# Optimization experiments

Measured on AMD Instinct MI355X. Metric: run time of the kernel, lower is better.

Reference implementation:

```python
import jax, jax.numpy as jnp
import numpy as np

N_NODES = 163840
N_EDGES = 2621440
F_IN = 64
F_HID = 64
SUBG = 20  # size_subgraph_samples
NEG_SLOPE = 0.2


def gat_conv(x, src, dst, W, a_src, a_dst, b):
    """PyG GATConv, heads=1, concat. src/dst already include self-loops."""
    n = x.shape[0]
    h = x @ W                               # [N, H]
    al_s = h @ a_src                        # [N]
    al_d = h @ a_dst                        # [N]
    e = jax.nn.leaky_relu(al_s[src] + al_d[dst], NEG_SLOPE)  # [E]
    # softmax over incoming edges of each dst node
    m = jax.ops.segment_max(e, dst, num_segments=n)
    ex = jnp.exp(e - m[dst])
    denom = jax.ops.segment_sum(ex, dst, num_segments=n)
    alpha = ex / (denom[dst] + 1e-16)
    msg = h[src] * alpha[:, None]           # [E, H]
    out = jax.ops.segment_sum(msg, dst, num_segments=n)
    return out + b


def setup_inputs() -> dict:
    key = jax.random.key(0)
    ks = jax.random.split(key, 12)
    s = 0.05
    return {
        "x": jax.random.normal(ks[0], (N_NODES, F_IN), jnp.float32),
        "edge_index": jax.random.randint(ks[1], (2, N_EDGES), 0, N_NODES, jnp.int64 if jax.config.jax_enable_x64 else jnp.int32),
        "W1": jax.random.normal(ks[2], (F_IN, F_HID), jnp.float32) * s,
        "a_src1": jax.random.normal(ks[3], (F_HID,), jnp.float32) * s,
        "a_dst1": jax.random.normal(ks[4], (F_HID,), jnp.float32) * s,
        "b1": jnp.zeros((F_HID,), jnp.float32),
        "W2": jax.random.normal(ks[5], (F_HID, F_HID), jnp.float32) * s,
        "a_src2": jax.random.normal(ks[6], (F_HID,), jnp.float32) * s,
        "a_dst2": jax.random.normal(ks[7], (F_HID,), jnp.float32) * s,
        "b2": jnp.zeros((F_HID,), jnp.float32),
        "W_out": jax.random.normal(ks[8], (F_HID * SUBG, 1), jnp.float32) * s,
        "b_out": jnp.zeros((1,), jnp.float32),
    }


def reference(x, edge_index, W1, a_src1, a_dst1, b1, W2, a_src2, a_dst2, b2, W_out, b_out):
    n = x.shape[0]
    loop = jnp.arange(n, dtype=edge_index.dtype)
    src = jnp.concatenate([edge_index[0], loop])  # add_self_loops=True
    dst = jnp.concatenate([edge_index[1], loop])
    h = gat_conv(x, src, dst, W1, a_src1, a_dst1, b1)
    h = jax.nn.relu(h)  # dropout is identity in eval mode
    h = gat_conv(h, src, dst, W2, a_src2, a_dst2, b2)
    h = jax.nn.relu(h)
    h = h.reshape(n // SUBG, F_HID * SUBG)
    return h @ W_out + b_out
```

## Files before the change

kernel.cpp:

```cpp
#include <hip/hip_runtime.h>
#include <math.h>

#define F 64
#define NPB 160
#define STAGE_CAP 6304

typedef __attribute__((ext_vector_type(8))) short bf16x8;
typedef __attribute__((ext_vector_type(4))) float f32x4;

__device__ inline unsigned short f2bf(float f) {
  unsigned int u = __float_as_uint(f);
  u += 0x7fffu + ((u >> 16) & 1u);
  return (unsigned short)(u >> 16);
}


__global__ __launch_bounds__(256) void k_bin_count(const int* __restrict__ edst, int* __restrict__ cntT,
                                                   int e, int ch, int nblk, int nb,
                                                   const float* __restrict__ W1, const float* __restrict__ W2,
                                                   uint4* __restrict__ wf) {
  __shared__ int h[1024];
  int k = blockIdx.x, tid = threadIdx.x;
  if (k == nblk) {
    for (int i = tid; i < 1024; i += 256) {
      int layer = i >> 9, rem = i & 511;
      int cb = rem >> 6, lane = rem & 63;
      int c = cb >> 1, kk = cb & 1;
      int l15 = lane & 15, quad = lane >> 4;
      const float* W = layer ? W2 : W1;
      unsigned short p[8];
      #pragma unroll
      for (int j = 0; j < 8; j++) {
        int kd = kk * 32 + quad * 8 + j;
        p[j] = f2bf(W[kd * F + c * 16 + l15]);
      }
      wf[i] = *(const uint4*)p;
    }
    return;
  }
  for (int i = tid; i < nb; i += 256) h[i] = 0;
  __syncthreads();
  int beg = k * ch, end = min(e, beg + ch);
  for (int i = beg + tid; i < end; i += 256) atomicAdd(&h[edst[i] / NPB], 1);
  __syncthreads();
  for (int b = tid; b < nb; b += 256) cntT[b * nblk + k] = h[b];
}

__global__ __launch_bounds__(256) void k_scan1(const int* __restrict__ counts, int* __restrict__ offs,
                                               int* __restrict__ bsums, int n) {
  int tid = threadIdx.x, lane = tid & 63, wv = tid >> 6;
  int i = blockIdx.x * 256 + tid;
  int v = (i < n) ? counts[i] : 0;
  int x = v;
  #pragma unroll
  for (int o = 1; o <= 32; o <<= 1) { int y = __shfl_up(x, o); if (lane >= o) x += y; }
  __shared__ int wsum[4];
  if (lane == 63) wsum[wv] = x;
  __syncthreads();
  int add = 0;
  for (int w = 0; w < wv; w++) add += wsum[w];
  int incl = x + add;
  if (i < n) offs[i] = incl - v;
  if (tid == 255) bsums[blockIdx.x] = incl;
}

__global__ __launch_bounds__(256) void k_scan2(int* __restrict__ bs, int nb,
                                               float* __restrict__ out, const float* __restrict__ bo, int ng) {
  __shared__ int wsum[4];
  __shared__ int carry_sh;
  int tid = threadIdx.x, lane = tid & 63, wv = tid >> 6;
  float b0 = bo[0];
  for (int i = tid; i < ng; i += 256) out[i] = b0;
  if (tid == 0) carry_sh = 0;
  __syncthreads();
  for (int base = 0; base < nb; base += 256) {
    int i = base + tid;
    int v = (i < nb) ? bs[i] : 0;
    int x = v;
    #pragma unroll
    for (int o = 1; o <= 32; o <<= 1) { int y = __shfl_up(x, o); if (lane >= o) x += y; }
    if (lane == 63) wsum[wv] = x;
    __syncthreads();
    int add = 0;
    for (int w = 0; w < wv; w++) add += wsum[w];
    int incl = x + add;
    int carry = carry_sh;
    if (i < nb) bs[i] = incl - v + carry;
    __syncthreads();
    if (tid == 255) carry_sh = carry + incl;
    __syncthreads();
  }
}

__global__ __launch_bounds__(256) void k_bin_scatter(const int* __restrict__ esrc, const int* __restrict__ edst,
                                                     const int* __restrict__ posT, const int* __restrict__ bsums,
                                                     unsigned int* __restrict__ binned,
                                                     int e, int ch, int nblk, int nb) {
  __shared__ int cur[1024];
  int k = blockIdx.x, tid = threadIdx.x;
  for (int b = tid; b < nb; b += 256) {
    int idx = b * nblk + k;
    cur[b] = posT[idx] + bsums[idx >> 8];
  }
  __syncthreads();
  int beg = k * ch, end = min(e, beg + ch);
  for (int i = beg + tid; i < end; i += 256) {
    int d = edst[i];
    int b = d / NPB;
    unsigned int ld = (unsigned int)(d - b * NPB);
    int p = atomicAdd(&cur[b], 1);
    binned[p] = (unsigned int)esrc[i] | (ld << 24);
  }
}

__global__ __launch_bounds__(256) void k_bucket_csr(const unsigned int* __restrict__ binned,
                                                    const int* __restrict__ posT, const int* __restrict__ bsums,
                                                    int* __restrict__ ssrc, int* __restrict__ offs,
                                                    int n, int nblk, int nb, int e) {
  __shared__ int ncnt[NPB];
  __shared__ int noff[NPB];
  __shared__ int cur[NPB];
  __shared__ int sc[256];
  __shared__ int stage[STAGE_CAP];
  int b = blockIdx.x, tid = threadIdx.x;
  int node0 = b * NPB;
  int nn = min(NPB, n - node0);
  int i0 = b * nblk;
  int ebeg = posT[i0] + bsums[i0 >> 8];
  int eend;
  if (b == nb - 1) eend = e;
  else { int i1 = (b + 1) * nblk; eend = posT[i1] + bsums[i1 >> 8]; }
  int ecnt = eend - ebeg;
  for (int i = tid; i < NPB; i += 256) ncnt[i] = 0;
  __syncthreads();
  for (int i = tid; i < ecnt; i += 256) { unsigned int v = binned[ebeg + i]; atomicAdd(&ncnt[v >> 24], 1); }
  __syncthreads();
  int x = (tid < nn) ? ncnt[tid] + 1 : 0;
  sc[tid] = x;
  __syncthreads();
  #pragma unroll
  for (int o = 1; o < 256; o <<= 1) {
    int y = (tid >= o) ? sc[tid - o] : 0;
    __syncthreads();
    sc[tid] += y;
    __syncthreads();
  }
  if (tid < nn) noff[tid] = sc[tid] - x;
  __syncthreads();
  int tot = ecnt + nn;
  int outbase = ebeg + node0;
  bool staged = (tot <= STAGE_CAP);
  if (tid < nn) {
    cur[tid] = noff[tid] + 1;
    offs[node0 + tid] = outbase + noff[tid];
    if (staged) stage[noff[tid]] = node0 + tid;
    else        ssrc[outbase + noff[tid]] = node0 + tid;
  }
  __syncthreads();
  if (staged) {
    for (int i = tid; i < ecnt; i += 256) {
      unsigned int v = binned[ebeg + i];
      int p = atomicAdd(&cur[v >> 24], 1);
      stage[p] = (int)(v & 0xFFFFFFu);
    }
    __syncthreads();
    for (int i = tid; i < tot; i += 256) ssrc[outbase + i] = stage[i];
  } else {
    for (int i = tid; i < ecnt; i += 256) {
      unsigned int v = binned[ebeg + i];
      int p = atomicAdd(&cur[v >> 24], 1);
      ssrc[outbase + p] = (int)(v & 0xFFFFFFu);
    }
  }
  if (b == 0 && tid == 0) offs[n] = e + n;
}

template<bool IN_BF16>
__global__ __launch_bounds__(256) void k_gemm(const void* __restrict__ in, const uint4* __restrict__ wf,
                                              const float* __restrict__ avs, const float* __restrict__ avd,
                                              unsigned short* __restrict__ hgb, float* __restrict__ als,
                                              float* __restrict__ ald, int n) {
  int tid = threadIdx.x, lane = tid & 63, wv = tid >> 6;
  int l15 = lane & 15, quad = lane >> 4;
  bf16x8 bfr[4][2];
  #pragma unroll
  for (int cb = 0; cb < 8; cb++) {
    uint4 u = wf[cb * 64 + lane];
    bfr[cb >> 1][cb & 1] = *(const bf16x8*)&u;
  }
  float as_l[4], ad_l[4];
  #pragma unroll
  for (int c = 0; c < 4; c++) { as_l[c] = avs[c * 16 + l15]; ad_l[c] = avd[c * 16 + l15]; }

  int nchunks = n >> 6;
  for (int chunk = blockIdx.x; chunk < nchunks; chunk += gridDim.x) {
    int r0 = (chunk << 6) + (wv << 4);
    bf16x8 a0, a1;
    if constexpr (IN_BF16) {
      const uint4* row4 = (const uint4*)((const unsigned short*)in + (size_t)(r0 + l15) * F);
      uint4 u0 = row4[quad];
      uint4 u1 = row4[quad + 4];
      a0 = *(const bf16x8*)&u0;
      a1 = *(const bf16x8*)&u1;
    } else {
      const float4* xr = (const float4*)((const float*)in + (size_t)(r0 + l15) * F + quad * 8);
      float4 xa = xr[0], xb = xr[1];
      float4 xc = xr[8], xd = xr[9];
      a0[0] = (short)f2bf(xa.x); a0[1] = (short)f2bf(xa.y); a0[2] = (short)f2bf(xa.z); a0[3] = (short)f2bf(xa.w);
      a0[4] = (short)f2bf(xb.x); a0[5] = (short)f2bf(xb.y); a0[6] = (short)f2bf(xb.z); a0[7] = (short)f2bf(xb.w);
      a1[0] = (short)f2bf(xc.x); a1[1] = (short)f2bf(xc.y); a1[2] = (short)f2bf(xc.z); a1[3] = (short)f2bf(xc.w);
      a1[4] = (short)f2bf(xd.x); a1[5] = (short)f2bf(xd.y); a1[6] = (short)f2bf(xd.z); a1[7] = (short)f2bf(xd.w);
    }
    f32x4 cfr[4];
    #pragma unroll
    for (int c = 0; c < 4; c++) {
      cfr[c] = (f32x4){0.f, 0.f, 0.f, 0.f};
      cfr[c] = __builtin_amdgcn_mfma_f32_16x16x32_bf16(a0, bfr[c][0], cfr[c], 0, 0, 0);
      cfr[c] = __builtin_amdgcn_mfma_f32_16x16x32_bf16(a1, bfr[c][1], cfr[c], 0, 0, 0);
    }
    #pragma unroll
    for (int i = 0; i < 4; i++) {
      int row = r0 + quad * 4 + i;
      #pragma unroll
      for (int c = 0; c < 4; c++) hgb[(size_t)row * F + c * 16 + l15] = f2bf(cfr[c][i]);
      float ps = cfr[0][i] * as_l[0] + cfr[1][i] * as_l[1] + cfr[2][i] * as_l[2] + cfr[3][i] * as_l[3];
      float pd = cfr[0][i] * ad_l[0] + cfr[1][i] * ad_l[1] + cfr[2][i] * ad_l[2] + cfr[3][i] * ad_l[3];
      #pragma unroll
      for (int o = 1; o <= 8; o <<= 1) { ps += __shfl_xor(ps, o); pd += __shfl_xor(pd, o); }
      if (l15 == 0) { als[row] = ps; ald[row] = pd; }
    }
  }
}

template<int MODE>
__global__ __launch_bounds__(256) void k_spmm(const int* __restrict__ offs, const int* __restrict__ ssrc,
                                              const unsigned short* __restrict__ hgb,
                                              const float* __restrict__ als, const float* __restrict__ ald,
                                              const float* __restrict__ bias, const float* __restrict__ Wout,
                                              void* __restrict__ outp, int n) {
  int tid = threadIdx.x, lane = tid & 63, wv = tid >> 6;
  int g8 = lane >> 3, l8 = lane & 7;
  const uint4* hg4 = (const uint4*)hgb;
  float4 bl0 = ((const float4*)bias)[l8 * 2];
  float4 bl1 = ((const float4*)bias)[l8 * 2 + 1];

  int node = (blockIdx.x * 4 + wv) * 8 + g8;
  int cnode = min(node, n - 1);
  bool nodeok = node < n;
  int beg = offs[cnode];
  int deg = nodeok ? (offs[cnode + 1] - beg) : 0;
  int degc = max(deg - 1, 0);
  float aldv = ald[cnode];

  int dm = deg;
  #pragma unroll
  for (int o = 8; o <= 32; o <<= 1) dm = max(dm, __shfl_xor(dm, o));

  float s = 0.f;
  float acc[8];
  #pragma unroll
  for (int k = 0; k < 8; k++) acc[k] = 0.f;

  #pragma unroll 2
  for (int j = 0; j < dm; j++) {
    int jj = min(j, degc);
    int src = ssrc[beg + jj];
    float t = als[src] + aldv;
    t = fmaxf(t, 0.2f * t);
    float ex = (j < deg) ? __expf(t) : 0.f;
    s += ex;
    uint4 u = hg4[(size_t)src * 8 + l8];
    acc[0] = fmaf(ex, __uint_as_float(u.x << 16), acc[0]);
    acc[1] = fmaf(ex, __uint_as_float(u.x & 0xffff0000u), acc[1]);
    acc[2] = fmaf(ex, __uint_as_float(u.y << 16), acc[2]);
    acc[3] = fmaf(ex, __uint_as_float(u.y & 0xffff0000u), acc[3]);
    acc[4] = fmaf(ex, __uint_as_float(u.z << 16), acc[4]);
    acc[5] = fmaf(ex, __uint_as_float(u.z & 0xffff0000u), acc[5]);
    acc[6] = fmaf(ex, __uint_as_float(u.w << 16), acc[6]);
    acc[7] = fmaf(ex, __uint_as_float(u.w & 0xffff0000u), acc[7]);
  }

  if (!nodeok) return;
  float iv = 1.f / (s + 1e-16f);
  float r[8];
  r[0] = fmaxf(fmaf(acc[0], iv, bl0.x), 0.f);
  r[1] = fmaxf(fmaf(acc[1], iv, bl0.y), 0.f);
  r[2] = fmaxf(fmaf(acc[2], iv, bl0.z), 0.f);
  r[3] = fmaxf(fmaf(acc[3], iv, bl0.w), 0.f);
  r[4] = fmaxf(fmaf(acc[4], iv, bl1.x), 0.f);
  r[5] = fmaxf(fmaf(acc[5], iv, bl1.y), 0.f);
  r[6] = fmaxf(fmaf(acc[6], iv, bl1.z), 0.f);
  r[7] = fmaxf(fmaf(acc[7], iv, bl1.w), 0.f);
  if constexpr (MODE == 0) {
    unsigned short p[8];
    #pragma unroll
    for (int k = 0; k < 8; k++) p[k] = f2bf(r[k]);
    ((uint4*)outp)[(size_t)node * 8 + l8] = *(const uint4*)p;
  } else {
    int grp = node / 20, slot = node - grp * 20;
    const float* wr = Wout + slot * F + l8 * 8;
    float dot = 0.f;
    #pragma unroll
    for (int k = 0; k < 8; k++) dot = fmaf(r[k], wr[k], dot);
    #pragma unroll
    for (int o = 1; o <= 4; o <<= 1) dot += __shfl_xor(dot, o);
    if (l8 == 0) atomicAdd((float*)outp + grp, dot);
  }
}

extern "C" void kernel_launch(void* const* d_in, const int* in_sizes, int n_in,
                              void* d_out, int out_size, void* d_ws, size_t ws_size,
                              hipStream_t stream) {
  const float* x   = (const float*)d_in[0];
  const int*   ei  = (const int*)d_in[1];
  const float* W1  = (const float*)d_in[2];
  const float* as1 = (const float*)d_in[3];
  const float* ad1 = (const float*)d_in[4];
  const float* b1  = (const float*)d_in[5];
  const float* W2  = (const float*)d_in[6];
  const float* as2 = (const float*)d_in[7];
  const float* ad2 = (const float*)d_in[8];
  const float* b2  = (const float*)d_in[9];
  const float* Wo  = (const float*)d_in[10];
  const float* bo  = (const float*)d_in[11];
  float* out = (float*)d_out;

  const int N = in_sizes[0] / F;
  const int E = in_sizes[1] / 2;
  const int* esrc = ei;
  const int* edst = ei + E;

  size_t off = 0;
  auto alloc = [&](size_t bytes) -> void* {
    void* p = (char*)d_ws + off;
    off += (bytes + 255) & ~(size_t)255;
    return p;
  };
  float* A    = (float*)alloc((size_t)N * F * 4);
  unsigned short* hgb = (unsigned short*)alloc((size_t)N * F * 2);
  float* als  = (float*)alloc((size_t)N * 4);
  float* ald  = (float*)alloc((size_t)N * 4);
  int* offs   = (int*)alloc((size_t)(N + 1) * 4);
  int* bsums  = (int*)alloc(8192);
  int* ssrc   = (int*)alloc((size_t)(E + N) * 4);
  uint4* wf   = (uint4*)alloc(16384);
  (void)ws_size; (void)n_in; (void)out_size;

  const int NBLK = 256;
  const int NB = (N + NPB - 1) / NPB;
  const int CH = (E + NBLK - 1) / NBLK;
  const int FLAT = NB * NBLK;

  int* cntT = (int*)A;
  int* posT = (int*)((char*)A + ((size_t)FLAT * 4 + 1024));
  unsigned int* binned = (unsigned int*)hgb;

  int gF = (FLAT + 255) / 256;
  int NG = N / 20;

  k_bin_count<<<NBLK + 1, 256, 0, stream>>>(edst, cntT, E, CH, NBLK, NB, W1, W2, wf);
  k_scan1<<<gF, 256, 0, stream>>>(cntT, posT, bsums, FLAT);
  k_scan2<<<1, 256, 0, stream>>>(bsums, gF, out, bo, NG);
  k_bin_scatter<<<NBLK, 256, 0, stream>>>(esrc, edst, posT, bsums, binned, E, CH, NBLK, NB);
  k_bucket_csr<<<NB, 256, 0, stream>>>(binned, posT, bsums, ssrc, offs, N, NBLK, NB, E);

  int gSp = (N + 31) / 32;
  k_gemm<false><<<2560, 256, 0, stream>>>(x, wf, as1, ad1, hgb, als, ald, N);
  k_spmm<0><<<gSp, 256, 0, stream>>>(offs, ssrc, hgb, als, ald, b1, nullptr, A, N);
  k_gemm<true><<<2560, 256, 0, stream>>>(A, wf + 512, as2, ad2, hgb, als, ald, N);
  k_spmm<1><<<gSp, 256, 0, stream>>>(offs, ssrc, hgb, als, ald, b2, Wo, out, N);
}
```

Measured before the change: 319.6 us.

## Fuse layer-1 GEMM into bin scatter and aggregate output atomics in shared memory

The layer-1 feature GEMM now runs in the same launch as the edge bin-scatter: the first blocks scatter edges and the extra blocks compute the GEMM. The binned edge buffer moves out of hgb into a separate region of A so the two can run side by side. The final SpMM sums the Wout dot products per subgraph group in shared memory before issuing a few global atomics, instead of one global atomic per node. The GEMM grids are also resized to one block per 64-row chunk. This removes a kernel launch and most global atomics, at the cost of extra block syncs and a dependence on the new buffer layout fitting inside A.

```diff
diff --git a/kernel.cpp b/kernel.cpp
--- a/kernel.cpp
+++ b/kernel.cpp
@@ -92,25 +92,97 @@
   }
 }
 
-__global__ __launch_bounds__(256) void k_bin_scatter(const int* __restrict__ esrc, const int* __restrict__ edst,
-                                                     const int* __restrict__ posT, const int* __restrict__ bsums,
-                                                     unsigned int* __restrict__ binned,
-                                                     int e, int ch, int nblk, int nb) {
-  __shared__ int cur[1024];
+template<bool IN_BF16>
+__device__ __forceinline__ void gemm_body(const void* __restrict__ in, const uint4* __restrict__ wf,
+                                          const float* __restrict__ avs, const float* __restrict__ avd,
+                                          unsigned short* __restrict__ hgb, float* __restrict__ als,
+                                          float* __restrict__ ald, int n, int bid, int nbl) {
+  int tid = threadIdx.x, lane = tid & 63, wv = tid >> 6;
+  int l15 = lane & 15, quad = lane >> 4;
+  bf16x8 bfr[4][2];
+  #pragma unroll
+  for (int cb = 0; cb < 8; cb++) {
+    uint4 u = wf[cb * 64 + lane];
+    bfr[cb >> 1][cb & 1] = *(const bf16x8*)&u;
+  }
+  float as_l[4], ad_l[4];
+  #pragma unroll
+  for (int c = 0; c < 4; c++) { as_l[c] = avs[c * 16 + l15]; ad_l[c] = avd[c * 16 + l15]; }
+
+  int nchunks = n >> 6;
+  for (int chunk = bid; chunk < nchunks; chunk += nbl) {
+    int r0 = (chunk << 6) + (wv << 4);
+    bf16x8 a0, a1;
+    if constexpr (IN_BF16) {
+      const uint4* row4 = (const uint4*)((const unsigned short*)in + (size_t)(r0 + l15) * F);
+      uint4 u0 = row4[quad];
+      uint4 u1 = row4[quad + 4];
+      a0 = *(const bf16x8*)&u0;
+      a1 = *(const bf16x8*)&u1;
+    } else {
+      const float4* xr = (const float4*)((const float*)in + (size_t)(r0 + l15) * F + quad * 8);
+      float4 xa = xr[0], xb = xr[1];
+      float4 xc = xr[8], xd = xr[9];
+      a0[0] = (short)f2bf(xa.x); a0[1] = (short)f2bf(xa.y); a0[2] = (short)f2bf(xa.z); a0[3] = (short)f2bf(xa.w);
+      a0[4] = (short)f2bf(xb.x); a0[5] = (short)f2bf(xb.y); a0[6] = (short)f2bf(xb.z); a0[7] = (short)f2bf(xb.w);
+      a1[0] = (short)f2bf(xc.x); a1[1] = (short)f2bf(xc.y); a1[2] = (short)f2bf(xc.z); a1[3] = (short)f2bf(xc.w);
+      a1[4] = (short)f2bf(xd.x); a1[5] = (short)f2bf(xd.y); a1[6] = (short)f2bf(xd.z); a1[7] = (short)f2bf(xd.w);
+    }
+    f32x4 cfr[4];
+    #pragma unroll
+    for (int c = 0; c < 4; c++) {
+      cfr[c] = (f32x4){0.f, 0.f, 0.f, 0.f};
+      cfr[c] = __builtin_amdgcn_mfma_f32_16x16x32_bf16(a0, bfr[c][0], cfr[c], 0, 0, 0);
+      cfr[c] = __builtin_amdgcn_mfma_f32_16x16x32_bf16(a1, bfr[c][1], cfr[c], 0, 0, 0);
+    }
+    #pragma unroll
+    for (int i = 0; i < 4; i++) {
+      int row = r0 + quad * 4 + i;
+      #pragma unroll
+      for (int c = 0; c < 4; c++) hgb[(size_t)row * F + c * 16 + l15] = f2bf(cfr[c][i]);
+      float ps = cfr[0][i] * as_l[0] + cfr[1][i] * as_l[1] + cfr[2][i] * as_l[2] + cfr[3][i] * as_l[3];
+      float pd = cfr[0][i] * ad_l[0] + cfr[1][i] * ad_l[1] + cfr[2][i] * ad_l[2] + cfr[3][i] * ad_l[3];
+      #pragma unroll
+      for (int o = 1; o <= 8; o <<= 1) { ps += __shfl_xor(ps, o); pd += __shfl_xor(pd, o); }
+      if (l15 == 0) { als[row] = ps; ald[row] = pd; }
+    }
+  }
+}
+
+__global__ __launch_bounds__(256) void k_scatter_gemm1(const int* __restrict__ esrc, const int* __restrict__ edst,
+                                                       const int* __restrict__ posT, const int* __restrict__ bsums,
+                                                       unsigned int* __restrict__ binned,
+                                                       int e, int ch, int nblk, int nb,
+                                                       const float* __restrict__ x, const uint4* __restrict__ wf,
+                                                       const float* __restrict__ avs, const float* __restrict__ avd,
+                                                       unsigned short* __restrict__ hgb, float* __restrict__ als,
+                                                       float* __restrict__ ald, int n) {
   int k = blockIdx.x, tid = threadIdx.x;
-  for (int b = tid; b < nb; b += 256) {
-    int idx = b * nblk + k;
-    cur[b] = posT[idx] + bsums[idx >> 8];
-  }
-  __syncthreads();
-  int beg = k * ch, end = min(e, beg + ch);
-  for (int i = beg + tid; i < end; i += 256) {
-    int d = edst[i];
-    int b = d / NPB;
-    unsigned int ld = (unsigned int)(d - b * NPB);
-    int p = atomicAdd(&cur[b], 1);
-    binned[p] = (unsigned int)esrc[i] | (ld << 24);
-  }
+  if (k < nblk) {
+    __shared__ int cur[1024];
+    for (int b = tid; b < nb; b += 256) {
+      int idx = b * nblk + k;
+      cur[b] = posT[idx] + bsums[idx >> 8];
+    }
+    __syncthreads();
+    int beg = k * ch, end = min(e, beg + ch);
+    for (int i = beg + tid; i < end; i += 256) {
+      int d = edst[i];
+      int b = d / NPB;
+      unsigned int ld = (unsigned int)(d - b * NPB);
+      int p = atomicAdd(&cur[b], 1);
+      binned[p] = (unsigned int)esrc[i] | (ld << 24);
+    }
+    return;
+  }
+  gemm_body<false>(x, wf, avs, avd, hgb, als, ald, n, k - nblk, (int)gridDim.x - nblk);
+}
+
+__global__ __launch_bounds__(256) void k_gemm2(const unsigned short* __restrict__ in, const uint4* __restrict__ wf,
+                                               const float* __restrict__ avs, const float* __restrict__ avd,
+                                               unsigned short* __restrict__ hgb, float* __restrict__ als,
+                                               float* __restrict__ ald, int n) {
+  gemm_body<true>(in, wf, avs, avd, hgb, als, ald, n, blockIdx.x, gridDim.x);
 }
 
 __global__ __launch_bounds__(256) void k_bucket_csr(const unsigned int* __restrict__ binned,
@@ -175,63 +247,6 @@
   if (b == 0 && tid == 0) offs[n] = e + n;
 }
 
-template<bool IN_BF16>
-__global__ __launch_bounds__(256) void k_gemm(const void* __restrict__ in, const uint4* __restrict__ wf,
-                                              const float* __restrict__ avs, const float* __restrict__ avd,
-                                              unsigned short* __restrict__ hgb, float* __restrict__ als,
-                                              float* __restrict__ ald, int n) {
-  int tid = threadIdx.x, lane = tid & 63, wv = tid >> 6;
-  int l15 = lane & 15, quad = lane >> 4;
-  bf16x8 bfr[4][2];
-  #pragma unroll
-  for (int cb = 0; cb < 8; cb++) {
-    uint4 u = wf[cb * 64 + lane];
-    bfr[cb >> 1][cb & 1] = *(const bf16x8*)&u;
-  }
-  float as_l[4], ad_l[4];
-  #pragma unroll
-  for (int c = 0; c < 4; c++) { as_l[c] = avs[c * 16 + l15]; ad_l[c] = avd[c * 16 + l15]; }
-
-  int nchunks = n >> 6;
-  for (int chunk = blockIdx.x; chunk < nchunks; chunk += gridDim.x) {
-    int r0 = (chunk << 6) + (wv << 4);
-    bf16x8 a0, a1;
-    if constexpr (IN_BF16) {
-      const uint4* row4 = (const uint4*)((const unsigned short*)in + (size_t)(r0 + l15) * F);
-      uint4 u0 = row4[quad];
-      uint4 u1 = row4[quad + 4];
-      a0 = *(const bf16x8*)&u0;
-      a1 = *(const bf16x8*)&u1;
-    } else {
-      const float4* xr = (const float4*)((const float*)in + (size_t)(r0 + l15) * F + quad * 8);
-      float4 xa = xr[0], xb = xr[1];
-      float4 xc = xr[8], xd = xr[9];
-      a0[0] = (short)f2bf(xa.x); a0[1] = (short)f2bf(xa.y); a0[2] = (short)f2bf(xa.z); a0[3] = (short)f2bf(xa.w);
-      a0[4] = (short)f2bf(xb.x); a0[5] = (short)f2bf(xb.y); a0[6] = (short)f2bf(xb.z); a0[7] = (short)f2bf(xb.w);
-      a1[0] = (short)f2bf(xc.x); a1[1] = (short)f2bf(xc.y); a1[2] = (short)f2bf(xc.z); a1[3] = (short)f2bf(xc.w);
-      a1[4] = (short)f2bf(xd.x); a1[5] = (short)f2bf(xd.y); a1[6] = (short)f2bf(xd.z); a1[7] = (short)f2bf(xd.w);
-    }
-    f32x4 cfr[4];
-    #pragma unroll
-    for (int c = 0; c < 4; c++) {
-      cfr[c] = (f32x4){0.f, 0.f, 0.f, 0.f};
-      cfr[c] = __builtin_amdgcn_mfma_f32_16x16x32_bf16(a0, bfr[c][0], cfr[c], 0, 0, 0);
-      cfr[c] = __builtin_amdgcn_mfma_f32_16x16x32_bf16(a1, bfr[c][1], cfr[c], 0, 0, 0);
-    }
-    #pragma unroll
-    for (int i = 0; i < 4; i++) {
-      int row = r0 + quad * 4 + i;
-      #pragma unroll
-      for (int c = 0; c < 4; c++) hgb[(size_t)row * F + c * 16 + l15] = f2bf(cfr[c][i]);
-      float ps = cfr[0][i] * as_l[0] + cfr[1][i] * as_l[1] + cfr[2][i] * as_l[2] + cfr[3][i] * as_l[3];
-      float pd = cfr[0][i] * ad_l[0] + cfr[1][i] * ad_l[1] + cfr[2][i] * ad_l[2] + cfr[3][i] * ad_l[3];
-      #pragma unroll
-      for (int o = 1; o <= 8; o <<= 1) { ps += __shfl_xor(ps, o); pd += __shfl_xor(pd, o); }
-      if (l15 == 0) { als[row] = ps; ald[row] = pd; }
-    }
-  }
-}
-
 template<int MODE>
 __global__ __launch_bounds__(256) void k_spmm(const int* __restrict__ offs, const int* __restrict__ ssrc,
                                               const unsigned short* __restrict__ hgb,
@@ -243,6 +258,9 @@
   const uint4* hg4 = (const uint4*)hgb;
   float4 bl0 = ((const float4*)bias)[l8 * 2];
   float4 bl1 = ((const float4*)bias)[l8 * 2 + 1];
+
+  __shared__ float gsl[3];
+  if (MODE == 1 && tid < 3) gsl[tid] = 0.f;
 
   int node = (blockIdx.x * 4 + wv) * 8 + g8;
   int cnode = min(node, n - 1);
@@ -280,7 +298,6 @@
     acc[7] = fmaf(ex, __uint_as_float(u.w & 0xffff0000u), acc[7]);
   }
 
-  if (!nodeok) return;
   float iv = 1.f / (s + 1e-16f);
   float r[8];
   r[0] = fmaxf(fmaf(acc[0], iv, bl0.x), 0.f);
@@ -291,20 +308,30 @@
   r[5] = fmaxf(fmaf(acc[5], iv, bl1.y), 0.f);
   r[6] = fmaxf(fmaf(acc[6], iv, bl1.z), 0.f);
   r[7] = fmaxf(fmaf(acc[7], iv, bl1.w), 0.f);
+
   if constexpr (MODE == 0) {
+    if (!nodeok) return;
     unsigned short p[8];
     #pragma unroll
     for (int k = 0; k < 8; k++) p[k] = f2bf(r[k]);
     ((uint4*)outp)[(size_t)node * 8 + l8] = *(const uint4*)p;
   } else {
-    int grp = node / 20, slot = node - grp * 20;
+    int node0 = blockIdx.x * 32;
+    int grp0 = node0 / 20;
+    int grp = cnode / 20, slot = cnode - grp * 20;
     const float* wr = Wout + slot * F + l8 * 8;
     float dot = 0.f;
     #pragma unroll
     for (int k = 0; k < 8; k++) dot = fmaf(r[k], wr[k], dot);
     #pragma unroll
     for (int o = 1; o <= 4; o <<= 1) dot += __shfl_xor(dot, o);
-    if (l8 == 0) atomicAdd((float*)outp + grp, dot);
+    __syncthreads();
+    if (nodeok && l8 == 0) atomicAdd(&gsl[grp - grp0], dot);
+    __syncthreads();
+    if (tid < 3) {
+      float v = gsl[tid];
+      if (v != 0.f) atomicAdd((float*)outp + grp0 + tid, v);
+    }
   }
 }
 
@@ -353,7 +380,7 @@
 
   int* cntT = (int*)A;
   int* posT = (int*)((char*)A + ((size_t)FLAT * 4 + 1024));
-  unsigned int* binned = (unsigned int*)hgb;
+  unsigned int* binned = (unsigned int*)((char*)A + (size_t)8 * 1024 * 1024);
 
   int gF = (FLAT + 255) / 256;
   int NG = N / 20;
@@ -361,12 +388,12 @@
   k_bin_count<<<NBLK + 1, 256, 0, stream>>>(edst, cntT, E, CH, NBLK, NB, W1, W2, wf);
   k_scan1<<<gF, 256, 0, stream>>>(cntT, posT, bsums, FLAT);
   k_scan2<<<1, 256, 0, stream>>>(bsums, gF, out, bo, NG);
-  k_bin_scatter<<<NBLK, 256, 0, stream>>>(esrc, edst, posT, bsums, binned, E, CH, NBLK, NB);
+  k_scatter_gemm1<<<NBLK + (N >> 6), 256, 0, stream>>>(esrc, edst, posT, bsums, binned, E, CH, NBLK, NB,
+                                                       x, wf, as1, ad1, hgb, als, ald, N);
   k_bucket_csr<<<NB, 256, 0, stream>>>(binned, posT, bsums, ssrc, offs, N, NBLK, NB, E);
 
   int gSp = (N + 31) / 32;
-  k_gemm<false><<<2560, 256, 0, stream>>>(x, wf, as1, ad1, hgb, als, ald, N);
   k_spmm<0><<<gSp, 256, 0, stream>>>(offs, ssrc, hgb, als, ald, b1, nullptr, A, N);
-  k_gemm<true><<<2560, 256, 0, stream>>>(A, wf + 512, as2, ad2, hgb, als, ald, N);
+  k_gemm2<<<(N >> 6), 256, 0, stream>>>((const unsigned short*)A, wf + 512, as2, ad2, hgb, als, ald, N);
   k_spmm<1><<<gSp, 256, 0, stream>>>(offs, ssrc, hgb, als, ald, b2, Wo, out, N);
 }
```

Result: faster. 309.8 us (-3.1%).
